# Kernel optimization log

Measured on AMD Instinct MI355X. Metric: run time of the kernel, lower is better.

The kernel has to match this reference:

```python
import jax, jax.numpy as jnp
import numpy as np

N_NODES = 50000
N_EDGES = 600000
N_GRAPHS = 500


def gcn_conv(x, src, dst, W, b, n_nodes):
    # PyG GCNConv: add self-loops, symmetric normalization D^-1/2 (A+I) D^-1/2, then XW + b
    h = x @ W  # [N, F_out]
    loop = jnp.arange(n_nodes)
    s = jnp.concatenate([src, loop])
    d = jnp.concatenate([dst, loop])
    deg = jax.ops.segment_sum(jnp.ones_like(d, dtype=h.dtype), d, num_segments=n_nodes)
    dinv = jnp.where(deg > 0, jax.lax.rsqrt(jnp.maximum(deg, 1.0)), 0.0)
    norm = dinv[s] * dinv[d]  # [E+N]
    msg = h[s] * norm[:, None]  # gather + scale
    out = jax.ops.segment_sum(msg, d, num_segments=n_nodes)  # scatter-add
    return out + b


def setup_inputs() -> dict:
    key = jax.random.key(0)
    ks = jax.random.split(key, 12)
    F_in, H, Hf, D_out = 128, 128, 64, 1
    x = jax.random.normal(ks[0], (N_NODES, F_in), dtype=jnp.float32)
    edge_index = jax.random.randint(ks[1], (2, N_EDGES), 0, N_NODES, dtype=jnp.int64)
    batch = jnp.sort(jax.random.randint(ks[2], (N_NODES,), 0, N_GRAPHS, dtype=jnp.int64))
    def glorot(k, shape):
        lim = np.sqrt(6.0 / (shape[0] + shape[1]))
        return jax.random.uniform(k, shape, jnp.float32, -lim, lim)
    return {
        "x": x, "edge_index": edge_index, "batch": batch,
        "W1": glorot(ks[3], (F_in, H)), "b1": jnp.zeros((H,), jnp.float32),
        "W2": glorot(ks[4], (H, H)), "b2": jnp.zeros((H,), jnp.float32),
        "W3": glorot(ks[5], (H, H)), "b3": jnp.zeros((H,), jnp.float32),
        "Wf1": glorot(ks[6], (H, Hf)), "bf1": jnp.zeros((Hf,), jnp.float32),
        "Wf2": glorot(ks[7], (Hf, D_out)), "bf2": jnp.zeros((D_out,), jnp.float32),
    }


def reference(x, edge_index, batch, W1, b1, W2, b2, W3, b3, Wf1, bf1, Wf2, bf2):
    src, dst = edge_index[0], edge_index[1]
    n = x.shape[0]
    h = jax.nn.relu(gcn_conv(x, src, dst, W1, b1, n))
    h = jax.nn.relu(gcn_conv(h, src, dst, W2, b2, n))
    h = jax.nn.relu(gcn_conv(h, src, dst, W3, b3, n))
    # global_mean_pool: segment mean over graphs
    sums = jax.ops.segment_sum(h, batch, num_segments=N_GRAPHS)
    cnts = jax.ops.segment_sum(jnp.ones((n,), h.dtype), batch, num_segments=N_GRAPHS)
    hg = sums / jnp.maximum(cnts, 1.0)[:, None]  # [G, 128]
    h = jax.nn.relu(hg @ Wf1 + bf1)
    return h @ Wf2 + bf2
```

## Files before the change

### kernel.cpp

```cpp
#include <hip/hip_runtime.h>

#define N_NODES 50000
#define N_EDGES 600000
#define N_GRAPHS 500
#define F 128

typedef short bf16x8 __attribute__((ext_vector_type(8)));
typedef float f32x4 __attribute__((ext_vector_type(4)));
union U4H8 { uint4 u; bf16x8 h; };

__device__ inline unsigned pk_bf16(float a, float b) {
    unsigned ua = __float_as_uint(a), ub = __float_as_uint(b);
    ua = (ua + 0x7fffu + ((ua >> 16) & 1u)) >> 16;
    ub = (ub + 0x7fffu + ((ub >> 16) & 1u)) >> 16;
    return ua | (ub << 16);
}
__device__ inline float bf16_rnd(float x) {
    unsigned u = __float_as_uint(x);
    u = (u + 0x7fffu + ((u >> 16) & 1u)) & 0xffff0000u;
    return __uint_as_float(u);
}
__device__ inline unsigned short bf16_1(float a) {
    unsigned ua = __float_as_uint(a);
    return (unsigned short)((ua + 0x7fffu + ((ua >> 16) & 1u)) >> 16);
}
#define BF_LO(u) __uint_as_float((u) << 16)
#define BF_HI(u) __uint_as_float((u) & 0xffff0000u)

__global__ __launch_bounds__(256) void k_hist(const int* __restrict__ dst, int* __restrict__ cnt, int ne) {
    int e = blockIdx.x * 256 + threadIdx.x;
    if (e < ne) atomicAdd(&cnt[dst[e]], 1);
}

__global__ __launch_bounds__(256) void k_scan1(const int* __restrict__ cnt, int* __restrict__ row_ptr,
                                               int* __restrict__ blksums, float* __restrict__ dinv, int n) {
    __shared__ int s[256];
    int i = blockIdx.x * 256 + threadIdx.x;
    int v = (i < n) ? cnt[i] : 0;
    if (i < n) dinv[i] = rsqrtf((float)(v + 1));
    s[threadIdx.x] = v;
    __syncthreads();
    for (int off = 1; off < 256; off <<= 1) {
        int t = (threadIdx.x >= off) ? s[threadIdx.x - off] : 0;
        __syncthreads();
        s[threadIdx.x] += t;
        __syncthreads();
    }
    if (i < n) row_ptr[i] = s[threadIdx.x] - v;
    if (threadIdx.x == 255) blksums[blockIdx.x] = s[255];
}

__global__ __launch_bounds__(256) void k_scan2(int* __restrict__ blksums, int nb) {
    __shared__ int s[256];
    int v = (threadIdx.x < nb) ? blksums[threadIdx.x] : 0;
    s[threadIdx.x] = v;
    __syncthreads();
    for (int off = 1; off < 256; off <<= 1) {
        int t = (threadIdx.x >= off) ? s[threadIdx.x - off] : 0;
        __syncthreads();
        s[threadIdx.x] += t;
        __syncthreads();
    }
    if (threadIdx.x < nb) blksums[threadIdx.x] = s[threadIdx.x] - v;
}

__global__ __launch_bounds__(256) void k_scan3(int* __restrict__ row_ptr, const int* __restrict__ blksums,
                                               int n, int ne) {
    int i = blockIdx.x * 256 + threadIdx.x;
    if (i < n) row_ptr[i] += blksums[blockIdx.x];
    if (i == 0) row_ptr[n] = ne;
}

__global__ __launch_bounds__(256) void k_fill(const int* __restrict__ src, const int* __restrict__ dst,
                                              const int* __restrict__ row_ptr, int* __restrict__ cnt,
                                              const float* __restrict__ dinv,
                                              int2* __restrict__ esw, int ne) {
    int e = blockIdx.x * 256 + threadIdx.x;
    if (e < ne) {
        int d = dst[e];
        int s = src[e];
        int pos = row_ptr[d] + atomicSub(&cnt[d], 1) - 1;
        esw[pos] = make_int2(s, __float_as_int(dinv[s]));
    }
}

__global__ __launch_bounds__(256) void k_prepW(const float* __restrict__ W1, const float* __restrict__ W2,
                                               const float* __restrict__ W3,
                                               uint4* __restrict__ Whi, uint4* __restrict__ Wlo) {
    int idx = blockIdx.x * 256 + threadIdx.x;
    int layer = idx >> 11;
    const float* W = (layer == 0) ? W1 : (layer == 1) ? W2 : W3;
    int t = idx & 2047;
    int lane = t & 63, sc = t >> 6;
    int s = sc >> 3, c = sc & 7;
    int q = lane >> 4, m = lane & 15;
    int k0 = 32 * s + 8 * q, n0 = 16 * c + m;
    float w[8], h[8];
    #pragma unroll
    for (int j = 0; j < 8; ++j) {
        w[j] = W[(k0 + j) * F + n0];
        h[j] = bf16_rnd(w[j]);
    }
    uint4 uh, ul;
    uh.x = pk_bf16(h[0], h[1]); uh.y = pk_bf16(h[2], h[3]);
    uh.z = pk_bf16(h[4], h[5]); uh.w = pk_bf16(h[6], h[7]);
    ul.x = pk_bf16(w[0] - h[0], w[1] - h[1]); ul.y = pk_bf16(w[2] - h[2], w[3] - h[3]);
    ul.z = pk_bf16(w[4] - h[4], w[5] - h[5]); ul.w = pk_bf16(w[6] - h[6], w[7] - h[7]);
    Whi[idx] = uh;
    Wlo[idx] = ul;
}

__global__ __launch_bounds__(256) void k_gemm_mfma(const float* __restrict__ X,
                                                   const uint4* __restrict__ Whi,
                                                   const uint4* __restrict__ Wlo,
                                                   unsigned short* __restrict__ Tb, int n_rows) {
    __shared__ uint4 Wl[4096];
    int tid = threadIdx.x;
    #pragma unroll
    for (int i = 0; i < 8; ++i) {
        Wl[tid + 256 * i] = Whi[tid + 256 * i];
        Wl[2048 + tid + 256 * i] = Wlo[tid + 256 * i];
    }
    __syncthreads();
    int wave = tid >> 6, lane = tid & 63;
    int q = lane >> 4, m = lane & 15;
    int rowA = blockIdx.x * 64 + wave * 16 + m;
    int rowAc = rowA < n_rows ? rowA : (n_rows - 1);
    f32x4 acc[8];
    #pragma unroll
    for (int c = 0; c < 8; ++c) acc[c] = (f32x4){0.f, 0.f, 0.f, 0.f};
    #pragma unroll
    for (int s = 0; s < 4; ++s) {
        const float* xr = X + (size_t)rowAc * F + 32 * s + 8 * q;
        float4 f0 = ((const float4*)xr)[0];
        float4 f1 = ((const float4*)xr)[1];
        float h0 = bf16_rnd(f0.x), h1 = bf16_rnd(f0.y), h2 = bf16_rnd(f0.z), h3 = bf16_rnd(f0.w);
        float h4 = bf16_rnd(f1.x), h5 = bf16_rnd(f1.y), h6 = bf16_rnd(f1.z), h7 = bf16_rnd(f1.w);
        U4H8 ahi, alo;
        ahi.u.x = (__float_as_uint(h0) >> 16) | (__float_as_uint(h1) & 0xffff0000u);
        ahi.u.y = (__float_as_uint(h2) >> 16) | (__float_as_uint(h3) & 0xffff0000u);
        ahi.u.z = (__float_as_uint(h4) >> 16) | (__float_as_uint(h5) & 0xffff0000u);
        ahi.u.w = (__float_as_uint(h6) >> 16) | (__float_as_uint(h7) & 0xffff0000u);
        alo.u.x = pk_bf16(f0.x - h0, f0.y - h1);
        alo.u.y = pk_bf16(f0.z - h2, f0.w - h3);
        alo.u.z = pk_bf16(f1.x - h4, f1.y - h5);
        alo.u.w = pk_bf16(f1.z - h6, f1.w - h7);
        #pragma unroll
        for (int c = 0; c < 8; ++c) {
            U4H8 bh, bl;
            bh.u = Wl[(s * 8 + c) * 64 + lane];
            bl.u = Wl[2048 + (s * 8 + c) * 64 + lane];
            acc[c] = __builtin_amdgcn_mfma_f32_16x16x32_bf16(ahi.h, bh.h, acc[c], 0, 0, 0);
            acc[c] = __builtin_amdgcn_mfma_f32_16x16x32_bf16(alo.h, bh.h, acc[c], 0, 0, 0);
            acc[c] = __builtin_amdgcn_mfma_f32_16x16x32_bf16(ahi.h, bl.h, acc[c], 0, 0, 0);
        }
    }
    int outr0 = blockIdx.x * 64 + wave * 16 + 4 * q;
    #pragma unroll
    for (int c = 0; c < 8; ++c) {
        #pragma unroll
        for (int r = 0; r < 4; ++r) {
            int rr = outr0 + r;
            if (rr < n_rows) Tb[(size_t)rr * F + 16 * c + m] = bf16_1(acc[c][r]);
        }
    }
}

__global__ __launch_bounds__(256) void k_gather(const int* __restrict__ row_ptr,
                                                const int2* __restrict__ esw,
                                                const float* __restrict__ dinv,
                                                const unsigned short* __restrict__ Tb,
                                                const float* __restrict__ bias,
                                                float* __restrict__ H, int n) {
    int grp = threadIdx.x >> 4;
    int node = blockIdx.x * 16 + grp;
    if (node >= n) return;
    int sub = threadIdx.x & 15;
    int beg = row_ptr[node], end = row_ptr[node + 1];
    float dd = dinv[node];

    float4 accL = make_float4(0.f, 0.f, 0.f, 0.f);
    float4 accH = make_float4(0.f, 0.f, 0.f, 0.f);

    for (int chunk = beg; chunk <= end; chunk += 16) {
        int e = chunk + sub;
        int2 rec;
        if (e < end)       rec = esw[e];
        else if (e == end) rec = make_int2(node, __float_as_int(dd));
        else               rec = make_int2(node, 0);

        uint4 rows[16];
        #pragma unroll
        for (int j = 0; j < 16; ++j) {
            int sj = __shfl(rec.x, j, 16);
            rows[j] = ((const uint4*)(Tb + (size_t)sj * F))[sub];
        }
        #pragma unroll
        for (int j = 0; j < 16; ++j) {
            float wj = __uint_as_float((unsigned)__shfl(rec.y, j, 16)) * dd;
            accL.x = fmaf(BF_LO(rows[j].x), wj, accL.x);
            accL.y = fmaf(BF_HI(rows[j].x), wj, accL.y);
            accL.z = fmaf(BF_LO(rows[j].y), wj, accL.z);
            accL.w = fmaf(BF_HI(rows[j].y), wj, accL.w);
            accH.x = fmaf(BF_LO(rows[j].z), wj, accH.x);
            accH.y = fmaf(BF_HI(rows[j].z), wj, accH.y);
            accH.z = fmaf(BF_LO(rows[j].w), wj, accH.z);
            accH.w = fmaf(BF_HI(rows[j].w), wj, accH.w);
        }
    }

    const float4* bb = (const float4*)(bias + sub * 8);
    float4 b0 = bb[0], b1 = bb[1];
    float4 r0, r1;
    r0.x = fmaxf(accL.x + b0.x, 0.f);
    r0.y = fmaxf(accL.y + b0.y, 0.f);
    r0.z = fmaxf(accL.z + b0.z, 0.f);
    r0.w = fmaxf(accL.w + b0.w, 0.f);
    r1.x = fmaxf(accH.x + b1.x, 0.f);
    r1.y = fmaxf(accH.y + b1.y, 0.f);
    r1.z = fmaxf(accH.z + b1.z, 0.f);
    r1.w = fmaxf(accH.w + b1.w, 0.f);
    float4* op = (float4*)(H + (size_t)node * F + sub * 8);
    op[0] = r0;
    op[1] = r1;
}

__global__ __launch_bounds__(256) void k_pool_fc(const float* __restrict__ H,
                                                 const int* __restrict__ batch,
                                                 const float* __restrict__ Wf1,
                                                 const float* __restrict__ bf1,
                                                 const float* __restrict__ Wf2,
                                                 const float* __restrict__ bf2,
                                                 float* __restrict__ out) {
    int g = blockIdx.x;
    int tid = threadIdx.x;
    int lo = 0, hi = N_NODES;
    while (lo < hi) { int mid = (lo + hi) >> 1; if (batch[mid] < g) lo = mid + 1; else hi = mid; }
    int start = lo;
    hi = N_NODES;
    while (lo < hi) { int mid = (lo + hi) >> 1; if (batch[mid] <= g) lo = mid + 1; else hi = mid; }
    int end = lo;

    __shared__ float hs[4][F];
    __shared__ float hg[F];
    int wv = tid >> 6, lane = tid & 63;
    int half = lane >> 5, sub = lane & 31;
    float4 a = make_float4(0.f, 0.f, 0.f, 0.f);
    for (int i = start + wv * 2 + half; i < end; i += 8) {
        float4 v = ((const float4*)(H + (size_t)i * F))[sub];
        a.x += v.x; a.y += v.y; a.z += v.z; a.w += v.w;
    }
    a.x += __shfl_xor(a.x, 32, 64);
    a.y += __shfl_xor(a.y, 32, 64);
    a.z += __shfl_xor(a.z, 32, 64);
    a.w += __shfl_xor(a.w, 32, 64);
    if (half == 0) ((float4*)hs[wv])[sub] = a;
    __syncthreads();
    if (tid < F) {
        float inv = 1.0f / (float)((end - start) > 0 ? (end - start) : 1);
        hg[tid] = (hs[0][tid] + hs[1][tid] + hs[2][tid] + hs[3][tid]) * inv;
    }
    __syncthreads();
    if (tid < 64) {
        float acc = bf1[tid];
        #pragma unroll 4
        for (int f = 0; f < F; ++f) acc = fmaf(hg[f], Wf1[f * 64 + tid], acc);
        float v = fmaxf(acc, 0.f) * Wf2[tid];
        #pragma unroll
        for (int off = 32; off > 0; off >>= 1) v += __shfl_down(v, off, 64);
        if (tid == 0) out[g] = v + bf2[0];
    }
}

extern "C" void kernel_launch(void* const* d_in, const int* in_sizes, int n_in,
                              void* d_out, int out_size, void* d_ws, size_t ws_size,
                              hipStream_t stream) {
    const float* x    = (const float*)d_in[0];
    const int* eidx   = (const int*)d_in[1];
    const int* batch  = (const int*)d_in[2];
    const float* W1   = (const float*)d_in[3];
    const float* b1   = (const float*)d_in[4];
    const float* W2   = (const float*)d_in[5];
    const float* b2   = (const float*)d_in[6];
    const float* W3   = (const float*)d_in[7];
    const float* b3   = (const float*)d_in[8];
    const float* Wf1  = (const float*)d_in[9];
    const float* bf1  = (const float*)d_in[10];
    const float* Wf2  = (const float*)d_in[11];
    const float* bf2  = (const float*)d_in[12];
    float* out = (float*)d_out;

    const int* src = eidx;
    const int* dst = eidx + N_EDGES;

    char* p = (char*)d_ws;
    unsigned short* Tb = (unsigned short*)p;  p += (size_t)N_NODES * F * 2;
    float* Ha   = (float*)p;   p += (size_t)N_NODES * F * sizeof(float);
    float* Hc   = (float*)p;   p += (size_t)N_NODES * F * sizeof(float);
    int2* esw   = (int2*)p;    p += (size_t)N_EDGES * sizeof(int2);
    uint4* Whi  = (uint4*)p;   p += (size_t)3 * 2048 * sizeof(uint4);
    uint4* Wlo  = (uint4*)p;   p += (size_t)3 * 2048 * sizeof(uint4);
    float* dinv = (float*)p;   p += (size_t)N_NODES * sizeof(float);
    int* cnt     = (int*)p;    p += (size_t)N_NODES * sizeof(int);
    int* row_ptr = (int*)p;    p += (size_t)(N_NODES + 1) * sizeof(int);
    int* blksums = (int*)p;    p += 256 * sizeof(int);

    dim3 b256(256);
    int gNodes   = (N_NODES + 255) / 256;
    int gEdges   = (N_EDGES + 255) / 256;
    int gGemm    = (N_NODES + 63) / 64;
    int gGather  = (N_NODES + 15) / 16;

    k_prepW<<<24, b256, 0, stream>>>(W1, W2, W3, Whi, Wlo);

    hipMemsetAsync(cnt, 0, (size_t)N_NODES * sizeof(int), stream);
    k_hist<<<gEdges, b256, 0, stream>>>(dst, cnt, N_EDGES);
    k_scan1<<<gNodes, b256, 0, stream>>>(cnt, row_ptr, blksums, dinv, N_NODES);
    k_scan2<<<1, b256, 0, stream>>>(blksums, gNodes);
    k_scan3<<<gNodes, b256, 0, stream>>>(row_ptr, blksums, N_NODES, N_EDGES);
    k_fill<<<gEdges, b256, 0, stream>>>(src, dst, row_ptr, cnt, dinv, esw, N_EDGES);

    k_gemm_mfma<<<gGemm, b256, 0, stream>>>(x, Whi, Wlo, Tb, N_NODES);
    k_gather<<<gGather, b256, 0, stream>>>(row_ptr, esw, dinv, Tb, b1, Ha, N_NODES);

    k_gemm_mfma<<<gGemm, b256, 0, stream>>>(Ha, Whi + 2048, Wlo + 2048, Tb, N_NODES);
    k_gather<<<gGather, b256, 0, stream>>>(row_ptr, esw, dinv, Tb, b2, Hc, N_NODES);

    k_gemm_mfma<<<gGemm, b256, 0, stream>>>(Hc, Whi + 4096, Wlo + 4096, Tb, N_NODES);
    k_gather<<<gGather, b256, 0, stream>>>(row_ptr, esw, dinv, Tb, b3, Ha, N_NODES);

    k_pool_fc<<<N_GRAPHS, b256, 0, stream>>>(Ha, batch, Wf1, bf1, Wf2, bf2, out);
}
```

Measured before the change: 301.3 us.

## Fuse aggregation with next-layer GEMM and store hidden activations in bf16

Layers 2 and 3 now aggregate neighbour rows first and apply the weight matrix afterwards, using (A·H)W = A·(HW). The aggregated tile sits in shared memory and feeds a split hi/lo bf16 MFMA GEMM inside one kernel, so the intermediate T buffer no longer makes a round trip through global memory. Hidden activations are stored as bf16 instead of fp32, which halves write and pooling read traffic. In exchange, each 64-node block runs a serial gather loop over 4 nodes per thread group, which may lower parallelism and hurt load balance, and the bf16 activations add rounding error.

```diff
diff --git a/kernel.cpp b/kernel.cpp
--- a/kernel.cpp
+++ b/kernel.cpp
@@ -171,7 +171,7 @@
                                                 const float* __restrict__ dinv,
                                                 const unsigned short* __restrict__ Tb,
                                                 const float* __restrict__ bias,
-                                                float* __restrict__ H, int n) {
+                                                unsigned short* __restrict__ Hb, int n) {
     int grp = threadIdx.x >> 4;
     int node = blockIdx.x * 16 + grp;
     if (node >= n) return;
@@ -211,21 +211,127 @@
 
     const float4* bb = (const float4*)(bias + sub * 8);
     float4 b0 = bb[0], b1 = bb[1];
-    float4 r0, r1;
-    r0.x = fmaxf(accL.x + b0.x, 0.f);
-    r0.y = fmaxf(accL.y + b0.y, 0.f);
-    r0.z = fmaxf(accL.z + b0.z, 0.f);
-    r0.w = fmaxf(accL.w + b0.w, 0.f);
-    r1.x = fmaxf(accH.x + b1.x, 0.f);
-    r1.y = fmaxf(accH.y + b1.y, 0.f);
-    r1.z = fmaxf(accH.z + b1.z, 0.f);
-    r1.w = fmaxf(accH.w + b1.w, 0.f);
-    float4* op = (float4*)(H + (size_t)node * F + sub * 8);
-    op[0] = r0;
-    op[1] = r1;
-}
-
-__global__ __launch_bounds__(256) void k_pool_fc(const float* __restrict__ H,
+    uint4 o;
+    o.x = pk_bf16(fmaxf(accL.x + b0.x, 0.f), fmaxf(accL.y + b0.y, 0.f));
+    o.y = pk_bf16(fmaxf(accL.z + b0.z, 0.f), fmaxf(accL.w + b0.w, 0.f));
+    o.z = pk_bf16(fmaxf(accH.x + b1.x, 0.f), fmaxf(accH.y + b1.y, 0.f));
+    o.w = pk_bf16(fmaxf(accH.z + b1.z, 0.f), fmaxf(accH.w + b1.w, 0.f));
+    ((uint4*)(Hb + (size_t)node * F))[sub] = o;
+}
+
+#define GP 132
+__global__ __launch_bounds__(256) void k_fused(const int* __restrict__ row_ptr,
+                                               const int2* __restrict__ esw,
+                                               const float* __restrict__ dinv,
+                                               const unsigned short* __restrict__ Hin,
+                                               const uint4* __restrict__ Whi,
+                                               const uint4* __restrict__ Wlo,
+                                               const float* __restrict__ bias,
+                                               unsigned short* __restrict__ Hout, int n) {
+    __shared__ float G[64 * GP];
+    int tid = threadIdx.x;
+    int d0 = blockIdx.x * 64;
+    int grp = tid >> 4, sub = tid & 15;
+
+    for (int i = 0; i < 4; ++i) {
+        int nl = 4 * grp + i;
+        int node = d0 + nl;
+        float4 accL = make_float4(0.f, 0.f, 0.f, 0.f);
+        float4 accH = make_float4(0.f, 0.f, 0.f, 0.f);
+        if (node < n) {
+            int beg = row_ptr[node], end = row_ptr[node + 1];
+            float dd = dinv[node];
+            for (int chunk = beg; chunk <= end; chunk += 16) {
+                int e = chunk + sub;
+                int2 rec;
+                if (e < end)       rec = esw[e];
+                else if (e == end) rec = make_int2(node, __float_as_int(dd));
+                else               rec = make_int2(node, 0);
+                uint4 rows[16];
+                #pragma unroll
+                for (int j = 0; j < 16; ++j) {
+                    int sj = __shfl(rec.x, j, 16);
+                    rows[j] = ((const uint4*)(Hin + (size_t)sj * F))[sub];
+                }
+                #pragma unroll
+                for (int j = 0; j < 16; ++j) {
+                    float wj = __uint_as_float((unsigned)__shfl(rec.y, j, 16)) * dd;
+                    accL.x = fmaf(BF_LO(rows[j].x), wj, accL.x);
+                    accL.y = fmaf(BF_HI(rows[j].x), wj, accL.y);
+                    accL.z = fmaf(BF_LO(rows[j].y), wj, accL.z);
+                    accL.w = fmaf(BF_HI(rows[j].y), wj, accL.w);
+                    accH.x = fmaf(BF_LO(rows[j].z), wj, accH.x);
+                    accH.y = fmaf(BF_HI(rows[j].z), wj, accH.y);
+                    accH.z = fmaf(BF_LO(rows[j].w), wj, accH.z);
+                    accH.w = fmaf(BF_HI(rows[j].w), wj, accH.w);
+                }
+            }
+            float* gr = &G[nl * GP + 8 * sub];
+            ((float4*)gr)[0] = accL;
+            ((float4*)gr)[1] = accH;
+        }
+    }
+    __syncthreads();
+
+    int wave = tid >> 6, lane = tid & 63;
+    int q = lane >> 4, m = lane & 15;
+    f32x4 acc[8];
+    #pragma unroll
+    for (int c = 0; c < 8; ++c) acc[c] = (f32x4){0.f, 0.f, 0.f, 0.f};
+    #pragma unroll
+    for (int s = 0; s < 4; ++s) {
+        const float* gr = &G[(16 * wave + m) * GP + 32 * s + 8 * q];
+        float4 f0 = ((const float4*)gr)[0];
+        float4 f1 = ((const float4*)gr)[1];
+        float h0 = bf16_rnd(f0.x), h1 = bf16_rnd(f0.y), h2 = bf16_rnd(f0.z), h3 = bf16_rnd(f0.w);
+        float h4 = bf16_rnd(f1.x), h5 = bf16_rnd(f1.y), h6 = bf16_rnd(f1.z), h7 = bf16_rnd(f1.w);
+        U4H8 ahi, alo;
+        ahi.u.x = (__float_as_uint(h0) >> 16) | (__float_as_uint(h1) & 0xffff0000u);
+        ahi.u.y = (__float_as_uint(h2) >> 16) | (__float_as_uint(h3) & 0xffff0000u);
+        ahi.u.z = (__float_as_uint(h4) >> 16) | (__float_as_uint(h5) & 0xffff0000u);
+        ahi.u.w = (__float_as_uint(h6) >> 16) | (__float_as_uint(h7) & 0xffff0000u);
+        alo.u.x = pk_bf16(f0.x - h0, f0.y - h1);
+        alo.u.y = pk_bf16(f0.z - h2, f0.w - h3);
+        alo.u.z = pk_bf16(f1.x - h4, f1.y - h5);
+        alo.u.w = pk_bf16(f1.z - h6, f1.w - h7);
+        #pragma unroll
+        for (int c = 0; c < 8; ++c) {
+            U4H8 bh, bl;
+            bh.u = Whi[(s * 8 + c) * 64 + lane];
+            bl.u = Wlo[(s * 8 + c) * 64 + lane];
+            acc[c] = __builtin_amdgcn_mfma_f32_16x16x32_bf16(ahi.h, bh.h, acc[c], 0, 0, 0);
+            acc[c] = __builtin_amdgcn_mfma_f32_16x16x32_bf16(alo.h, bh.h, acc[c], 0, 0, 0);
+            acc[c] = __builtin_amdgcn_mfma_f32_16x16x32_bf16(ahi.h, bl.h, acc[c], 0, 0, 0);
+        }
+    }
+    __syncthreads();
+
+    #pragma unroll
+    for (int c = 0; c < 8; ++c) {
+        float bb = bias[16 * c + m];
+        #pragma unroll
+        for (int r = 0; r < 4; ++r)
+            G[(16 * wave + 4 * q + r) * GP + 16 * c + m] = fmaxf(acc[c][r] + bb, 0.f);
+    }
+    __syncthreads();
+    #pragma unroll
+    for (int j = 0; j < 4; ++j) {
+        int lin = tid + 256 * j;
+        int row = lin >> 4, c8 = lin & 15;
+        int node = d0 + row;
+        if (node < n) {
+            const float* gr = &G[row * GP + c8 * 8];
+            uint4 o;
+            o.x = pk_bf16(gr[0], gr[1]);
+            o.y = pk_bf16(gr[2], gr[3]);
+            o.z = pk_bf16(gr[4], gr[5]);
+            o.w = pk_bf16(gr[6], gr[7]);
+            ((uint4*)(Hout + (size_t)node * F))[c8] = o;
+        }
+    }
+}
+
+__global__ __launch_bounds__(256) void k_pool_fc(const unsigned short* __restrict__ Hb,
                                                  const int* __restrict__ batch,
                                                  const float* __restrict__ Wf1,
                                                  const float* __restrict__ bf1,
@@ -247,8 +353,9 @@
     int half = lane >> 5, sub = lane & 31;
     float4 a = make_float4(0.f, 0.f, 0.f, 0.f);
     for (int i = start + wv * 2 + half; i < end; i += 8) {
-        float4 v = ((const float4*)(H + (size_t)i * F))[sub];
-        a.x += v.x; a.y += v.y; a.z += v.z; a.w += v.w;
+        uint2 v = ((const uint2*)(Hb + (size_t)i * F))[sub];
+        a.x += BF_LO(v.x); a.y += BF_HI(v.x);
+        a.z += BF_LO(v.y); a.w += BF_HI(v.y);
     }
     a.x += __shfl_xor(a.x, 32, 64);
     a.y += __shfl_xor(a.y, 32, 64);
@@ -294,9 +401,10 @@
     const int* dst = eidx + N_EDGES;
 
     char* p = (char*)d_ws;
-    unsigned short* Tb = (unsigned short*)p;  p += (size_t)N_NODES * F * 2;
-    float* Ha   = (float*)p;   p += (size_t)N_NODES * F * sizeof(float);
-    float* Hc   = (float*)p;   p += (size_t)N_NODES * F * sizeof(float);
+    unsigned short* Tb  = (unsigned short*)p;  p += (size_t)N_NODES * F * 2;
+    unsigned short* H1  = (unsigned short*)p;  p += (size_t)N_NODES * F * 2;
+    unsigned short* H2  = (unsigned short*)p;  p += (size_t)N_NODES * F * 2;
+    unsigned short* H3  = (unsigned short*)p;  p += (size_t)N_NODES * F * 2;
     int2* esw   = (int2*)p;    p += (size_t)N_EDGES * sizeof(int2);
     uint4* Whi  = (uint4*)p;   p += (size_t)3 * 2048 * sizeof(uint4);
     uint4* Wlo  = (uint4*)p;   p += (size_t)3 * 2048 * sizeof(uint4);
@@ -310,6 +418,7 @@
     int gEdges   = (N_EDGES + 255) / 256;
     int gGemm    = (N_NODES + 63) / 64;
     int gGather  = (N_NODES + 15) / 16;
+    int gFused   = (N_NODES + 63) / 64;
 
     k_prepW<<<24, b256, 0, stream>>>(W1, W2, W3, Whi, Wlo);
 
@@ -321,13 +430,11 @@
     k_fill<<<gEdges, b256, 0, stream>>>(src, dst, row_ptr, cnt, dinv, esw, N_EDGES);
 
     k_gemm_mfma<<<gGemm, b256, 0, stream>>>(x, Whi, Wlo, Tb, N_NODES);
-    k_gather<<<gGather, b256, 0, stream>>>(row_ptr, esw, dinv, Tb, b1, Ha, N_NODES);
-
-    k_gemm_mfma<<<gGemm, b256, 0, stream>>>(Ha, Whi + 2048, Wlo + 2048, Tb, N_NODES);
-    k_gather<<<gGather, b256, 0, stream>>>(row_ptr, esw, dinv, Tb, b2, Hc, N_NODES);
-
-    k_gemm_mfma<<<gGemm, b256, 0, stream>>>(Hc, Whi + 4096, Wlo + 4096, Tb, N_NODES);
-    k_gather<<<gGather, b256, 0, stream>>>(row_ptr, esw, dinv, Tb, b3, Ha, N_NODES);
-
-    k_pool_fc<<<N_GRAPHS, b256, 0, stream>>>(Ha, batch, Wf1, bf1, Wf2, bf2, out);
-}
+    k_gather<<<gGather, b256, 0, stream>>>(row_ptr, esw, dinv, Tb, b1, H1, N_NODES);
+
+    k_fused<<<gFused, b256, 0, stream>>>(row_ptr, esw, dinv, H1, Whi + 2048, Wlo + 2048, b2, H2, N_NODES);
+
+    k_fused<<<gFused, b256, 0, stream>>>(row_ptr, esw, dinv, H2, Whi + 4096, Wlo + 4096, b3, H3, N_NODES);
+
+    k_pool_fc<<<N_GRAPHS, b256, 0, stream>>>(H3, batch, Wf1, bf1, Wf2, bf2, out);
+}
```

Measured after the change: 296.1 us. No clear change (-1.7%).

## Fuse aggregate-then-transform GCN layers and store activations in bf16

Applied to the files above, without the earlier changes.

Reorders each GCN layer to aggregate neighbours first, (A·X)·W instead of A·(X·W). The gather and the MFMA GEMM now run in one kernel per layer, with the aggregated tile staged in shared memory. Activations between layers are kept as bf16 rather than fp32, and the input is converted to bf16 once up front. This removes the separate GEMM launches and the fp32 activation round trips. In exchange it adds extra bf16 rounding of the input and hidden states, and W is now read from global memory per block instead of being staged in LDS.

```diff
diff --git a/kernel.cpp b/kernel.cpp
--- a/kernel.cpp
+++ b/kernel.cpp
@@ -20,12 +20,21 @@
     u = (u + 0x7fffu + ((u >> 16) & 1u)) & 0xffff0000u;
     return __uint_as_float(u);
 }
-__device__ inline unsigned short bf16_1(float a) {
-    unsigned ua = __float_as_uint(a);
-    return (unsigned short)((ua + 0x7fffu + ((ua >> 16) & 1u)) >> 16);
-}
 #define BF_LO(u) __uint_as_float((u) << 16)
 #define BF_HI(u) __uint_as_float((u) & 0xffff0000u)
+
+__global__ __launch_bounds__(256) void k_cvt(const float* __restrict__ x,
+                                             unsigned short* __restrict__ xb, int n8) {
+    int idx = blockIdx.x * 256 + threadIdx.x;
+    if (idx < n8) {
+        const float4* xr = (const float4*)(x + (size_t)idx * 8);
+        float4 a = xr[0], b = xr[1];
+        uint4 o;
+        o.x = pk_bf16(a.x, a.y); o.y = pk_bf16(a.z, a.w);
+        o.z = pk_bf16(b.x, b.y); o.w = pk_bf16(b.z, b.w);
+        ((uint4*)xb)[idx] = o;
+    }
+}
 
 __global__ __launch_bounds__(256) void k_hist(const int* __restrict__ dst, int* __restrict__ cnt, int ne) {
     int e = blockIdx.x * 256 + threadIdx.x;
@@ -110,30 +119,75 @@
     Wlo[idx] = ul;
 }
 
-__global__ __launch_bounds__(256) void k_gemm_mfma(const float* __restrict__ X,
-                                                   const uint4* __restrict__ Whi,
-                                                   const uint4* __restrict__ Wlo,
-                                                   unsigned short* __restrict__ Tb, int n_rows) {
-    __shared__ uint4 Wl[4096];
+#define TN 32
+#define GP 132
+__global__ __launch_bounds__(256) void k_fused(const int* __restrict__ row_ptr,
+                                               const int2* __restrict__ esw,
+                                               const float* __restrict__ dinv,
+                                               const unsigned short* __restrict__ Hin,
+                                               const uint4* __restrict__ Whi,
+                                               const uint4* __restrict__ Wlo,
+                                               const float* __restrict__ bias,
+                                               unsigned short* __restrict__ Hout, int n) {
+    __shared__ float G[TN * GP];
     int tid = threadIdx.x;
-    #pragma unroll
-    for (int i = 0; i < 8; ++i) {
-        Wl[tid + 256 * i] = Whi[tid + 256 * i];
-        Wl[2048 + tid + 256 * i] = Wlo[tid + 256 * i];
-    }
-    __syncthreads();
+    int d0 = blockIdx.x * TN;
+    int grp = tid >> 4, sub = tid & 15;
+
+    #pragma unroll
+    for (int i = 0; i < 2; ++i) {
+        int nl = 2 * grp + i;
+        int node = d0 + nl;
+        float4 accL = make_float4(0.f, 0.f, 0.f, 0.f);
+        float4 accH = make_float4(0.f, 0.f, 0.f, 0.f);
+        if (node < n) {
+            int beg = row_ptr[node], end = row_ptr[node + 1];
+            float dd = dinv[node];
+            for (int chunk = beg; chunk <= end; chunk += 16) {
+                int e = chunk + sub;
+                int2 rec;
+                if (e < end)       rec = esw[e];
+                else if (e == end) rec = make_int2(node, __float_as_int(dd));
+                else               rec = make_int2(node, 0);
+                uint4 rows[16];
+                #pragma unroll
+                for (int j = 0; j < 16; ++j) {
+                    int sj = __shfl(rec.x, j, 16);
+                    rows[j] = ((const uint4*)(Hin + (size_t)sj * F))[sub];
+                }
+                #pragma unroll
+                for (int j = 0; j < 16; ++j) {
+                    float wj = __uint_as_float((unsigned)__shfl(rec.y, j, 16)) * dd;
+                    accL.x = fmaf(BF_LO(rows[j].x), wj, accL.x);
+                    accL.y = fmaf(BF_HI(rows[j].x), wj, accL.y);
+                    accL.z = fmaf(BF_LO(rows[j].y), wj, accL.z);
+                    accL.w = fmaf(BF_HI(rows[j].y), wj, accL.w);
+                    accH.x = fmaf(BF_LO(rows[j].z), wj, accH.x);
+                    accH.y = fmaf(BF_HI(rows[j].z), wj, accH.y);
+                    accH.z = fmaf(BF_LO(rows[j].w), wj, accH.z);
+                    accH.w = fmaf(BF_HI(rows[j].w), wj, accH.w);
+                }
+            }
+        }
+        float* gr = &G[nl * GP + 8 * sub];
+        ((float4*)gr)[0] = accL;
+        ((float4*)gr)[1] = accH;
+    }
+    __syncthreads();
+
     int wave = tid >> 6, lane = tid & 63;
     int q = lane >> 4, m = lane & 15;
-    int rowA = blockIdx.x * 64 + wave * 16 + m;
-    int rowAc = rowA < n_rows ? rowA : (n_rows - 1);
-    f32x4 acc[8];
-    #pragma unroll
-    for (int c = 0; c < 8; ++c) acc[c] = (f32x4){0.f, 0.f, 0.f, 0.f};
+    int rt = wave & 1;
+    int ch = (wave >> 1) * 4;
+    int row0 = 16 * rt;
+    f32x4 acc[4];
+    #pragma unroll
+    for (int c = 0; c < 4; ++c) acc[c] = (f32x4){0.f, 0.f, 0.f, 0.f};
     #pragma unroll
     for (int s = 0; s < 4; ++s) {
-        const float* xr = X + (size_t)rowAc * F + 32 * s + 8 * q;
-        float4 f0 = ((const float4*)xr)[0];
-        float4 f1 = ((const float4*)xr)[1];
+        const float* gr = &G[(row0 + m) * GP + 32 * s + 8 * q];
+        float4 f0 = ((const float4*)gr)[0];
+        float4 f1 = ((const float4*)gr)[1];
         float h0 = bf16_rnd(f0.x), h1 = bf16_rnd(f0.y), h2 = bf16_rnd(f0.z), h3 = bf16_rnd(f0.w);
         float h4 = bf16_rnd(f1.x), h5 = bf16_rnd(f1.y), h6 = bf16_rnd(f1.z), h7 = bf16_rnd(f1.w);
         U4H8 ahi, alo;
@@ -146,86 +200,45 @@
         alo.u.z = pk_bf16(f1.x - h4, f1.y - h5);
         alo.u.w = pk_bf16(f1.z - h6, f1.w - h7);
         #pragma unroll
-        for (int c = 0; c < 8; ++c) {
+        for (int cc = 0; cc < 4; ++cc) {
+            int c = ch + cc;
             U4H8 bh, bl;
-            bh.u = Wl[(s * 8 + c) * 64 + lane];
-            bl.u = Wl[2048 + (s * 8 + c) * 64 + lane];
-            acc[c] = __builtin_amdgcn_mfma_f32_16x16x32_bf16(ahi.h, bh.h, acc[c], 0, 0, 0);
-            acc[c] = __builtin_amdgcn_mfma_f32_16x16x32_bf16(alo.h, bh.h, acc[c], 0, 0, 0);
-            acc[c] = __builtin_amdgcn_mfma_f32_16x16x32_bf16(ahi.h, bl.h, acc[c], 0, 0, 0);
+            bh.u = Whi[(s * 8 + c) * 64 + lane];
+            bl.u = Wlo[(s * 8 + c) * 64 + lane];
+            acc[cc] = __builtin_amdgcn_mfma_f32_16x16x32_bf16(ahi.h, bh.h, acc[cc], 0, 0, 0);
+            acc[cc] = __builtin_amdgcn_mfma_f32_16x16x32_bf16(alo.h, bh.h, acc[cc], 0, 0, 0);
+            acc[cc] = __builtin_amdgcn_mfma_f32_16x16x32_bf16(ahi.h, bl.h, acc[cc], 0, 0, 0);
         }
     }
-    int outr0 = blockIdx.x * 64 + wave * 16 + 4 * q;
-    #pragma unroll
-    for (int c = 0; c < 8; ++c) {
+    __syncthreads();
+
+    #pragma unroll
+    for (int cc = 0; cc < 4; ++cc) {
+        int c = ch + cc;
+        float bb = bias[16 * c + m];
         #pragma unroll
-        for (int r = 0; r < 4; ++r) {
-            int rr = outr0 + r;
-            if (rr < n_rows) Tb[(size_t)rr * F + 16 * c + m] = bf16_1(acc[c][r]);
+        for (int r = 0; r < 4; ++r)
+            G[(row0 + 4 * q + r) * GP + 16 * c + m] = fmaxf(acc[cc][r] + bb, 0.f);
+    }
+    __syncthreads();
+    #pragma unroll
+    for (int j = 0; j < 2; ++j) {
+        int lin = tid + 256 * j;
+        int row = lin >> 4, c8 = lin & 15;
+        int node = d0 + row;
+        if (node < n) {
+            const float* gr = &G[row * GP + c8 * 8];
+            uint4 o;
+            o.x = pk_bf16(gr[0], gr[1]);
+            o.y = pk_bf16(gr[2], gr[3]);
+            o.z = pk_bf16(gr[4], gr[5]);
+            o.w = pk_bf16(gr[6], gr[7]);
+            ((uint4*)(Hout + (size_t)node * F))[c8] = o;
         }
     }
 }
 
-__global__ __launch_bounds__(256) void k_gather(const int* __restrict__ row_ptr,
-                                                const int2* __restrict__ esw,
-                                                const float* __restrict__ dinv,
-                                                const unsigned short* __restrict__ Tb,
-                                                const float* __restrict__ bias,
-                                                float* __restrict__ H, int n) {
-    int grp = threadIdx.x >> 4;
-    int node = blockIdx.x * 16 + grp;
-    if (node >= n) return;
-    int sub = threadIdx.x & 15;
-    int beg = row_ptr[node], end = row_ptr[node + 1];
-    float dd = dinv[node];
-
-    float4 accL = make_float4(0.f, 0.f, 0.f, 0.f);
-    float4 accH = make_float4(0.f, 0.f, 0.f, 0.f);
-
-    for (int chunk = beg; chunk <= end; chunk += 16) {
-        int e = chunk + sub;
-        int2 rec;
-        if (e < end)       rec = esw[e];
-        else if (e == end) rec = make_int2(node, __float_as_int(dd));
-        else               rec = make_int2(node, 0);
-
-        uint4 rows[16];
-        #pragma unroll
-        for (int j = 0; j < 16; ++j) {
-            int sj = __shfl(rec.x, j, 16);
-            rows[j] = ((const uint4*)(Tb + (size_t)sj * F))[sub];
-        }
-        #pragma unroll
-        for (int j = 0; j < 16; ++j) {
-            float wj = __uint_as_float((unsigned)__shfl(rec.y, j, 16)) * dd;
-            accL.x = fmaf(BF_LO(rows[j].x), wj, accL.x);
-            accL.y = fmaf(BF_HI(rows[j].x), wj, accL.y);
-            accL.z = fmaf(BF_LO(rows[j].y), wj, accL.z);
-            accL.w = fmaf(BF_HI(rows[j].y), wj, accL.w);
-            accH.x = fmaf(BF_LO(rows[j].z), wj, accH.x);
-            accH.y = fmaf(BF_HI(rows[j].z), wj, accH.y);
-            accH.z = fmaf(BF_LO(rows[j].w), wj, accH.z);
-            accH.w = fmaf(BF_HI(rows[j].w), wj, accH.w);
-        }
-    }
-
-    const float4* bb = (const float4*)(bias + sub * 8);
-    float4 b0 = bb[0], b1 = bb[1];
-    float4 r0, r1;
-    r0.x = fmaxf(accL.x + b0.x, 0.f);
-    r0.y = fmaxf(accL.y + b0.y, 0.f);
-    r0.z = fmaxf(accL.z + b0.z, 0.f);
-    r0.w = fmaxf(accL.w + b0.w, 0.f);
-    r1.x = fmaxf(accH.x + b1.x, 0.f);
-    r1.y = fmaxf(accH.y + b1.y, 0.f);
-    r1.z = fmaxf(accH.z + b1.z, 0.f);
-    r1.w = fmaxf(accH.w + b1.w, 0.f);
-    float4* op = (float4*)(H + (size_t)node * F + sub * 8);
-    op[0] = r0;
-    op[1] = r1;
-}
-
-__global__ __launch_bounds__(256) void k_pool_fc(const float* __restrict__ H,
+__global__ __launch_bounds__(256) void k_pool_fc(const unsigned short* __restrict__ Hb,
                                                  const int* __restrict__ batch,
                                                  const float* __restrict__ Wf1,
                                                  const float* __restrict__ bf1,
@@ -247,8 +260,9 @@
     int half = lane >> 5, sub = lane & 31;
     float4 a = make_float4(0.f, 0.f, 0.f, 0.f);
     for (int i = start + wv * 2 + half; i < end; i += 8) {
-        float4 v = ((const float4*)(H + (size_t)i * F))[sub];
-        a.x += v.x; a.y += v.y; a.z += v.z; a.w += v.w;
+        uint2 v = ((const uint2*)(Hb + (size_t)i * F))[sub];
+        a.x += BF_LO(v.x); a.y += BF_HI(v.x);
+        a.z += BF_LO(v.y); a.w += BF_HI(v.y);
     }
     a.x += __shfl_xor(a.x, 32, 64);
     a.y += __shfl_xor(a.y, 32, 64);
@@ -294,9 +308,10 @@
     const int* dst = eidx + N_EDGES;
 
     char* p = (char*)d_ws;
-    unsigned short* Tb = (unsigned short*)p;  p += (size_t)N_NODES * F * 2;
-    float* Ha   = (float*)p;   p += (size_t)N_NODES * F * sizeof(float);
-    float* Hc   = (float*)p;   p += (size_t)N_NODES * F * sizeof(float);
+    unsigned short* Xb  = (unsigned short*)p;  p += (size_t)N_NODES * F * 2;
+    unsigned short* H1  = (unsigned short*)p;  p += (size_t)N_NODES * F * 2;
+    unsigned short* H2  = (unsigned short*)p;  p += (size_t)N_NODES * F * 2;
+    unsigned short* H3  = (unsigned short*)p;  p += (size_t)N_NODES * F * 2;
     int2* esw   = (int2*)p;    p += (size_t)N_EDGES * sizeof(int2);
     uint4* Whi  = (uint4*)p;   p += (size_t)3 * 2048 * sizeof(uint4);
     uint4* Wlo  = (uint4*)p;   p += (size_t)3 * 2048 * sizeof(uint4);
@@ -306,11 +321,12 @@
     int* blksums = (int*)p;    p += 256 * sizeof(int);
 
     dim3 b256(256);
-    int gNodes   = (N_NODES + 255) / 256;
-    int gEdges   = (N_EDGES + 255) / 256;
-    int gGemm    = (N_NODES + 63) / 64;
-    int gGather  = (N_NODES + 15) / 16;
-
+    int gNodes = (N_NODES + 255) / 256;
+    int gEdges = (N_EDGES + 255) / 256;
+    int gCvt   = (N_NODES * F / 8 + 255) / 256;
+    int gFused = (N_NODES + TN - 1) / TN;
+
+    k_cvt<<<gCvt, b256, 0, stream>>>(x, Xb, N_NODES * F / 8);
     k_prepW<<<24, b256, 0, stream>>>(W1, W2, W3, Whi, Wlo);
 
     hipMemsetAsync(cnt, 0, (size_t)N_NODES * sizeof(int), stream);
@@ -320,14 +336,9 @@
     k_scan3<<<gNodes, b256, 0, stream>>>(row_ptr, blksums, N_NODES, N_EDGES);
     k_fill<<<gEdges, b256, 0, stream>>>(src, dst, row_ptr, cnt, dinv, esw, N_EDGES);
 
-    k_gemm_mfma<<<gGemm, b256, 0, stream>>>(x, Whi, Wlo, Tb, N_NODES);
-    k_gather<<<gGather, b256, 0, stream>>>(row_ptr, esw, dinv, Tb, b1, Ha, N_NODES);
-
-    k_gemm_mfma<<<gGemm, b256, 0, stream>>>(Ha, Whi + 2048, Wlo + 2048, Tb, N_NODES);
-    k_gather<<<gGather, b256, 0, stream>>>(row_ptr, esw, dinv, Tb, b2, Hc, N_NODES);
-
-    k_gemm_mfma<<<gGemm, b256, 0, stream>>>(Hc, Whi + 4096, Wlo + 4096, Tb, N_NODES);
-    k_gather<<<gGather, b256, 0, stream>>>(row_ptr, esw, dinv, Tb, b3, Ha, N_NODES);
-
-    k_pool_fc<<<N_GRAPHS, b256, 0, stream>>>(Ha, batch, Wf1, bf1, Wf2, bf2, out);
-}
+    k_fused<<<gFused, b256, 0, stream>>>(row_ptr, esw, dinv, Xb, Whi,        Wlo,        b1, H1, N_NODES);
+    k_fused<<<gFused, b256, 0, stream>>>(row_ptr, esw, dinv, H1, Whi + 2048, Wlo + 2048, b2, H2, N_NODES);
+    k_fused<<<gFused, b256, 0, stream>>>(row_ptr, esw, dinv, H2, Whi + 4096, Wlo + 4096, b3, H3, N_NODES);
+
+    k_pool_fc<<<N_GRAPHS, b256, 0, stream>>>(H3, batch, Wf1, bf1, Wf2, bf2, out);
+}
```

Measured after the change: 292.0 us. -3.1%, faster.
